# Optimization experiments

Measured on AMD Instinct MI355X. Metric: run time of the kernel, lower is better.

Reference implementation:

```python
import jax, jax.numpy as jnp
import numpy as np

T, B, I, H, O = 256, 64, 512, 1024, 256


def setup_inputs() -> dict:
    key = jax.random.key(0)
    ks = jax.random.split(key, 7)
    s_ih = 1.0 / np.sqrt(H)
    return {
        "x": jax.random.normal(ks[0], (T, B, I), dtype=jnp.float32),
        "W_ih": jax.random.uniform(ks[1], (4 * H, I), dtype=jnp.float32, minval=-s_ih, maxval=s_ih),
        "W_hh": jax.random.uniform(ks[2], (4 * H, H), dtype=jnp.float32, minval=-s_ih, maxval=s_ih),
        "b_ih": jax.random.uniform(ks[3], (4 * H,), dtype=jnp.float32, minval=-s_ih, maxval=s_ih),
        "b_hh": jax.random.uniform(ks[4], (4 * H,), dtype=jnp.float32, minval=-s_ih, maxval=s_ih),
        "fc_W": jax.random.uniform(ks[5], (O, H), dtype=jnp.float32, minval=-s_ih, maxval=s_ih),
        "fc_b": jax.random.uniform(ks[6], (O,), dtype=jnp.float32, minval=-s_ih, maxval=s_ih),
    }


def _lstm(x, W_ih, W_hh, b_ih, b_hh):
    # x: (T, B, I) seq-first, as PyTorch default. Gate order: i, f, g, o.
    Bsz = x.shape[1]
    Hh = W_hh.shape[1]
    # precompute input projections for all time steps: (T, B, 4H)
    xz = jnp.einsum('tbi,gi->tbg', x, W_ih) + b_ih + b_hh

    def step(carry, xz_t):
        h, c = carry
        z = xz_t + h @ W_hh.T  # (B, 4H)
        i, f, g, o = jnp.split(z, 4, axis=-1)
        i = jax.nn.sigmoid(i)
        f = jax.nn.sigmoid(f)
        g = jnp.tanh(g)
        o = jax.nn.sigmoid(o)
        c = f * c + i * g
        h = o * jnp.tanh(c)
        return (h, c), h

    h0 = jnp.zeros((Bsz, Hh), dtype=x.dtype)
    c0 = jnp.zeros((Bsz, Hh), dtype=x.dtype)
    _, hs = jax.lax.scan(step, (h0, c0), xz)
    return hs  # (T, B, H)


def reference(x, W_ih, W_hh, b_ih, b_hh, fc_W, fc_b):
    out = _lstm(x, W_ih, W_hh, b_ih, b_hh)  # (T, B, H)
    # Faithful to original: out[:, -1, :] indexes the LAST BATCH element
    # (seq-first layout), giving (T, H), then fc -> (T, O).
    last = out[:, -1, :]
    return last @ fc_W.T + fc_b
```

## Files before the change

kernel.cpp:

```cpp
#include <hip/hip_runtime.h>
#include <hip/hip_bf16.h>
#include <stdint.h>

#define T_STEPS 256
#define BATCH   64
#define IN_DIM  512
#define HID     1024
#define OUT_DIM 256
#define G4      4096
#define SENT    0x7FC07FC0u

__device__ __forceinline__ float bfbits2f(uint32_t b16) {
    return __uint_as_float(b16 << 16);
}
__device__ __forceinline__ uint32_t f2bfbits(float f) {
    uint32_t u = __float_as_uint(f);
    u += 0x7fffu + ((u >> 16) & 1u);
    return u >> 16;
}
__device__ __forceinline__ float fast_sigmoid(float x) {
    return 1.f / (1.f + __expf(-x));
}
__device__ __forceinline__ float fast_tanh(float x) {
    return 2.f / (1.f + __expf(-2.f * x)) - 1.f;
}

__global__ void init_sent(uint32_t* __restrict__ p, int n) {
    int i = blockIdx.x * 256 + threadIdx.x;
    if (i < n) p[i] = SENT;
}

template<bool ABF16>
__global__ __launch_bounds__(256) void gemm_bt(
    const void* __restrict__ Av, long lda,
    const float* __restrict__ Bw, int ldb,
    const float* __restrict__ bias1, const float* __restrict__ bias2,
    float* __restrict__ C, int ldc, int K)
{
    __shared__ float a_lds[64][68];
    __shared__ float w_lds[64][65];
    const int tid = threadIdx.x;
    const int m0 = blockIdx.y * 64, n0 = blockIdx.x * 64;
    const int kl = tid & 63, grp = tid >> 6;
    const int cc = tid & 31, r0 = (tid >> 5) * 8;

    float acc[16];
#pragma unroll
    for (int i = 0; i < 16; ++i) acc[i] = 0.f;

    for (int k0 = 0; k0 < K; k0 += 64) {
        __syncthreads();
#pragma unroll
        for (int i = 0; i < 16; ++i) {
            int r = grp + 4 * i;
            long ai = (long)(m0 + r) * lda + k0 + kl;
            float av = ABF16 ? bfbits2f(((const uint16_t*)Av)[ai])
                             : ((const float*)Av)[ai];
            a_lds[kl][r] = av;
            w_lds[kl][r] = Bw[(long)(n0 + r) * ldb + k0 + kl];
        }
        __syncthreads();
#pragma unroll 16
        for (int k = 0; k < 64; ++k) {
            float4 A0 = *(const float4*)&a_lds[k][r0];
            float4 A1 = *(const float4*)&a_lds[k][r0 + 4];
            float w0 = w_lds[k][cc], w1 = w_lds[k][cc + 32];
            float a[8] = {A0.x, A0.y, A0.z, A0.w, A1.x, A1.y, A1.z, A1.w};
#pragma unroll
            for (int i = 0; i < 8; ++i) {
                acc[i]     += a[i] * w0;
                acc[8 + i] += a[i] * w1;
            }
        }
    }
    float b0 = bias1[n0 + cc]      + (bias2 ? bias2[n0 + cc]      : 0.f);
    float b1 = bias1[n0 + cc + 32] + (bias2 ? bias2[n0 + cc + 32] : 0.f);
#pragma unroll
    for (int i = 0; i < 8; ++i) {
        C[(long)(m0 + r0 + i) * ldc + n0 + cc]      = acc[i]     + b0;
        C[(long)(m0 + r0 + i) * ldc + n0 + cc + 32] = acc[8 + i] + b1;
    }
}

__global__ __launch_bounds__(256) void lstm_rec(
    const float* __restrict__ W_hh,
    const float* __restrict__ xz,
    uint32_t* __restrict__ h_all)
{
    __shared__ float h_lds[HID];
    __shared__ float z_lds[16];

    const int g   = blockIdx.x;
    const int tid = threadIdx.x;
    const int kpart = tid & 15;
    const int row   = tid >> 4;
    const int gate  = row >> 2, ju = row & 3;
    const int grow  = gate * HID + g * 4 + ju;

    float w[64];
#pragma unroll
    for (int i = 0; i < 16; ++i) {
        int ch = (i + kpart) & 15;
        const float4 wv = *(const float4*)&W_hh[(long)grow * HID + kpart * 64 + ch * 4];
        w[4 * i + 0] = wv.x; w[4 * i + 1] = wv.y;
        w[4 * i + 2] = wv.z; w[4 * i + 3] = wv.w;
    }

    float c_state = 0.f;
    float xz_next = 0.f;
    if (kpart == 0) xz_next = xz[grow];

    for (int t = 0; t < T_STEPS; ++t) {
        if (t == 0) {
            float4 z4 = {0.f, 0.f, 0.f, 0.f};
            *(float4*)&h_lds[4 * tid] = z4;
        } else {
            const uint32_t* hsrc = h_all + (size_t)(t - 1) * 512;
            uint32_t v0, v1;
            do { v0 = __hip_atomic_load(&hsrc[2 * tid],     __ATOMIC_RELAXED, __HIP_MEMORY_SCOPE_AGENT); } while (v0 == SENT);
            do { v1 = __hip_atomic_load(&hsrc[2 * tid + 1], __ATOMIC_RELAXED, __HIP_MEMORY_SCOPE_AGENT); } while (v1 == SENT);
            float4 hv = { bfbits2f(v0 & 0xFFFFu), bfbits2f(v0 >> 16),
                          bfbits2f(v1 & 0xFFFFu), bfbits2f(v1 >> 16) };
            *(float4*)&h_lds[4 * tid] = hv;
        }
        __syncthreads();

        float xz_cur = 0.f;
        if (kpart == 0) {
            xz_cur = xz_next;
            int tn = (t + 1 < T_STEPS) ? t + 1 : t;
            xz_next = xz[(long)tn * G4 + grow];
        }

        float a0 = 0.f, a1 = 0.f, a2 = 0.f, a3 = 0.f;
#pragma unroll
        for (int i = 0; i < 16; ++i) {
            int ch = (i + kpart) & 15;
            float4 hv = *(const float4*)&h_lds[kpart * 64 + ch * 4];
            a0 += w[4 * i + 0] * hv.x;
            a1 += w[4 * i + 1] * hv.y;
            a2 += w[4 * i + 2] * hv.z;
            a3 += w[4 * i + 3] * hv.w;
        }
        float sum = (a0 + a1) + (a2 + a3);
        sum += __shfl_xor(sum, 1, 16);
        sum += __shfl_xor(sum, 2, 16);
        sum += __shfl_xor(sum, 4, 16);
        sum += __shfl_xor(sum, 8, 16);
        if (kpart == 0) z_lds[row] = sum + xz_cur;
        __syncthreads();

        if (tid < 4) {
            float zi = z_lds[tid], zf = z_lds[4 + tid];
            float zg = z_lds[8 + tid], zo = z_lds[12 + tid];
            float ii = fast_sigmoid(zi);
            float ff = fast_sigmoid(zf);
            float gg = fast_tanh(zg);
            float oo = fast_sigmoid(zo);
            c_state = ff * c_state + ii * gg;
            float h = oo * fast_tanh(c_state);
            uint32_t hb = f2bfbits(h);
            uint32_t other = __shfl_xor(hb, 1, 64);
            if ((tid & 1) == 0) {
                uint32_t dw = (hb & 0xFFFFu) | (other << 16);
                __hip_atomic_store(&h_all[(size_t)t * 512 + g * 2 + (tid >> 1)], dw,
                                   __ATOMIC_RELAXED, __HIP_MEMORY_SCOPE_AGENT);
            }
        }
    }
}

extern "C" void kernel_launch(void* const* d_in, const int* in_sizes, int n_in,
                              void* d_out, int out_size, void* d_ws, size_t ws_size,
                              hipStream_t stream) {
    const float* x    = (const float*)d_in[0];
    const float* W_ih = (const float*)d_in[1];
    const float* W_hh = (const float*)d_in[2];
    const float* b_ih = (const float*)d_in[3];
    const float* b_hh = (const float*)d_in[4];
    const float* fc_W = (const float*)d_in[5];
    const float* fc_b = (const float*)d_in[6];
    float* out = (float*)d_out;

    float*    xz    = (float*)d_ws;
    uint32_t* h_all = (uint32_t*)((char*)d_ws + (size_t)T_STEPS * G4 * 4);

    init_sent<<<(T_STEPS * HID / 2 + 255) / 256, 256, 0, stream>>>(h_all, T_STEPS * HID / 2);

    gemm_bt<false><<<dim3(G4 / 64, T_STEPS / 64), 256, 0, stream>>>(
        (const void*)(x + 63 * IN_DIM), (long)BATCH * IN_DIM,
        W_ih, IN_DIM, b_ih, b_hh, xz, G4, IN_DIM);

    lstm_rec<<<256, 256, 0, stream>>>(W_hh, xz, h_all);

    gemm_bt<true><<<dim3(OUT_DIM / 64, T_STEPS / 64), 256, 0, stream>>>(
        (const void*)h_all, HID, fc_W, HID, fc_b, nullptr, out, OUT_DIM, HID);
}
```

Baseline: 1.073 ms.

## Fuse input projection into recurrent kernel and tighten per-step sync

Removes the separate input-projection GEMM: each recurrent block computes its 16 gate rows of x·W_ih for all timesteps into LDS before the recurrence. Within each step, the gate sums are gathered with wave shuffles instead of a second __syncthreads, the h buffer is double-buffered, and each block writes its h values as individual 16-bit stores with cache-bypass bits. Consumers poll with one 64-bit load plus a sentinel check. This cuts one kernel launch, the xz round trip through global memory and a barrier per step, in exchange for redundant-free but serialized prologue work per block and stores that are not packed.

```diff
diff --git a/kernel.cpp b/kernel.cpp
--- a/kernel.cpp
+++ b/kernel.cpp
@@ -8,7 +8,8 @@
 #define HID     1024
 #define OUT_DIM 256
 #define G4      4096
-#define SENT    0x7FC07FC0u
+#define SENT32  0x7FC07FC0u
+#define SENT64  0x7FC07FC07FC07FC0ULL
 
 __device__ __forceinline__ float bfbits2f(uint32_t b16) {
     return __uint_as_float(b16 << 16);
@@ -24,17 +25,24 @@
 __device__ __forceinline__ float fast_tanh(float x) {
     return 2.f / (1.f + __expf(-2.f * x)) - 1.f;
 }
+__device__ __forceinline__ bool any_sent(uint64_t v) {
+    uint64_t x = v ^ SENT64;
+    return (((x - 0x0001000100010001ULL) & ~x) & 0x8000800080008000ULL) != 0ULL;
+}
+__device__ __forceinline__ uint64_t poll_load(const uint64_t* p) {
+    return __hip_atomic_load(p, __ATOMIC_RELAXED, __HIP_MEMORY_SCOPE_AGENT);
+}
 
 __global__ void init_sent(uint32_t* __restrict__ p, int n) {
     int i = blockIdx.x * 256 + threadIdx.x;
-    if (i < n) p[i] = SENT;
+    if (i < n) p[i] = SENT32;
 }
 
 template<bool ABF16>
 __global__ __launch_bounds__(256) void gemm_bt(
     const void* __restrict__ Av, long lda,
     const float* __restrict__ Bw, int ldb,
-    const float* __restrict__ bias1, const float* __restrict__ bias2,
+    const float* __restrict__ bias1,
     float* __restrict__ C, int ldc, int K)
 {
     __shared__ float a_lds[64][68];
@@ -73,8 +81,7 @@
             }
         }
     }
-    float b0 = bias1[n0 + cc]      + (bias2 ? bias2[n0 + cc]      : 0.f);
-    float b1 = bias1[n0 + cc + 32] + (bias2 ? bias2[n0 + cc + 32] : 0.f);
+    float b0 = bias1[n0 + cc], b1 = bias1[n0 + cc + 32];
 #pragma unroll
     for (int i = 0; i < 8; ++i) {
         C[(long)(m0 + r0 + i) * ldc + n0 + cc]      = acc[i]     + b0;
@@ -84,88 +91,126 @@
 
 __global__ __launch_bounds__(256) void lstm_rec(
     const float* __restrict__ W_hh,
-    const float* __restrict__ xz,
-    uint32_t* __restrict__ h_all)
+    const float* __restrict__ x,
+    const float* __restrict__ W_ih,
+    const float* __restrict__ b_ih,
+    const float* __restrict__ b_hh,
+    uint16_t* __restrict__ h_all)
 {
-    __shared__ float h_lds[HID];
-    __shared__ float z_lds[16];
-
-    const int g   = blockIdx.x;
-    const int tid = threadIdx.x;
+    __shared__ float h_lds[2][HID];
+    __shared__ float xz_lds[16][T_STEPS + 1];
+
+    const int g     = blockIdx.x;
+    const int tid   = threadIdx.x;
     const int kpart = tid & 15;
     const int row   = tid >> 4;
-    const int gate  = row >> 2, ju = row & 3;
+    const int ju    = row >> 2;
+    const int gate  = row & 3;
+    const int lane  = tid & 63;
     const int grow  = gate * HID + g * 4 + ju;
+
+    {
+        float wih[32];
+        const float* wp = W_ih + (long)grow * IN_DIM + kpart * 32;
+#pragma unroll
+        for (int i = 0; i < 8; ++i) {
+            float4 v = *(const float4*)(wp + 4 * i);
+            wih[4*i] = v.x; wih[4*i+1] = v.y; wih[4*i+2] = v.z; wih[4*i+3] = v.w;
+        }
+        float bsum = b_ih[grow] + b_hh[grow];
+        const float* xbase = x + (long)63 * IN_DIM + (long)kpart * 32;
+#pragma unroll 2
+        for (int t = 0; t < T_STEPS; ++t) {
+            const float* xp = xbase + (long)t * BATCH * IN_DIM;
+            float a0 = 0.f, a1 = 0.f, a2 = 0.f, a3 = 0.f;
+#pragma unroll
+            for (int i = 0; i < 8; ++i) {
+                float4 v = *(const float4*)(xp + 4 * i);
+                a0 += v.x * wih[4*i];   a1 += v.y * wih[4*i+1];
+                a2 += v.z * wih[4*i+2]; a3 += v.w * wih[4*i+3];
+            }
+            float acc = (a0 + a1) + (a2 + a3);
+            acc += __shfl_xor(acc, 1, 16);
+            acc += __shfl_xor(acc, 2, 16);
+            acc += __shfl_xor(acc, 4, 16);
+            acc += __shfl_xor(acc, 8, 16);
+            if (kpart == 0) xz_lds[row][t] = acc + bsum;
+        }
+    }
 
     float w[64];
 #pragma unroll
     for (int i = 0; i < 16; ++i) {
         int ch = (i + kpart) & 15;
-        const float4 wv = *(const float4*)&W_hh[(long)grow * HID + kpart * 64 + ch * 4];
-        w[4 * i + 0] = wv.x; w[4 * i + 1] = wv.y;
-        w[4 * i + 2] = wv.z; w[4 * i + 3] = wv.w;
-    }
+        float4 wv = *(const float4*)&W_hh[(long)grow * HID + kpart * 64 + ch * 4];
+        w[4*i] = wv.x; w[4*i+1] = wv.y; w[4*i+2] = wv.z; w[4*i+3] = wv.w;
+    }
+
+    {
+        float4 z4 = {0.f, 0.f, 0.f, 0.f};
+        *(float4*)&h_lds[0][4 * tid] = z4;
+    }
+    __syncthreads();
 
     float c_state = 0.f;
-    float xz_next = 0.f;
-    if (kpart == 0) xz_next = xz[grow];
+    float xz_next = xz_lds[row][0];
 
     for (int t = 0; t < T_STEPS; ++t) {
-        if (t == 0) {
-            float4 z4 = {0.f, 0.f, 0.f, 0.f};
-            *(float4*)&h_lds[4 * tid] = z4;
-        } else {
-            const uint32_t* hsrc = h_all + (size_t)(t - 1) * 512;
-            uint32_t v0, v1;
-            do { v0 = __hip_atomic_load(&hsrc[2 * tid],     __ATOMIC_RELAXED, __HIP_MEMORY_SCOPE_AGENT); } while (v0 == SENT);
-            do { v1 = __hip_atomic_load(&hsrc[2 * tid + 1], __ATOMIC_RELAXED, __HIP_MEMORY_SCOPE_AGENT); } while (v1 == SENT);
-            float4 hv = { bfbits2f(v0 & 0xFFFFu), bfbits2f(v0 >> 16),
-                          bfbits2f(v1 & 0xFFFFu), bfbits2f(v1 >> 16) };
-            *(float4*)&h_lds[4 * tid] = hv;
+        float* hb = h_lds[t & 1];
+        if (t > 0) {
+            const uint64_t* hsrc = (const uint64_t*)(h_all + (size_t)(t - 1) * HID);
+            uint64_t v = poll_load(&hsrc[tid]);
+            if (any_sent(v)) {
+                uint64_t a = poll_load(&hsrc[tid]);
+                uint64_t b = poll_load(&hsrc[tid]);
+                for (;;) {
+                    v = a; a = b; b = poll_load(&hsrc[tid]);
+                    if (!any_sent(v)) break;
+                }
+            }
+            float4 hv = { bfbits2f((uint32_t)(v        & 0xFFFFu)),
+                          bfbits2f((uint32_t)((v >> 16) & 0xFFFFu)),
+                          bfbits2f((uint32_t)((v >> 32) & 0xFFFFu)),
+                          bfbits2f((uint32_t)((v >> 48) & 0xFFFFu)) };
+            *(float4*)&hb[4 * tid] = hv;
         }
         __syncthreads();
 
-        float xz_cur = 0.f;
-        if (kpart == 0) {
-            xz_cur = xz_next;
-            int tn = (t + 1 < T_STEPS) ? t + 1 : t;
-            xz_next = xz[(long)tn * G4 + grow];
-        }
+        float xz_cur = xz_next;
+        int tn = (t + 1 < T_STEPS) ? t + 1 : t;
+        xz_next = xz_lds[row][tn];
 
         float a0 = 0.f, a1 = 0.f, a2 = 0.f, a3 = 0.f;
 #pragma unroll
         for (int i = 0; i < 16; ++i) {
-            int ch = (i + kpart) & 15;
-            float4 hv = *(const float4*)&h_lds[kpart * 64 + ch * 4];
-            a0 += w[4 * i + 0] * hv.x;
-            a1 += w[4 * i + 1] * hv.y;
-            a2 += w[4 * i + 2] * hv.z;
-            a3 += w[4 * i + 3] * hv.w;
+            float4 hv = *(const float4*)&hb[kpart * 64 + ((i + kpart) & 15) * 4];
+            a0 += w[4*i]   * hv.x;
+            a1 += w[4*i+1] * hv.y;
+            a2 += w[4*i+2] * hv.z;
+            a3 += w[4*i+3] * hv.w;
         }
         float sum = (a0 + a1) + (a2 + a3);
         sum += __shfl_xor(sum, 1, 16);
         sum += __shfl_xor(sum, 2, 16);
         sum += __shfl_xor(sum, 4, 16);
         sum += __shfl_xor(sum, 8, 16);
-        if (kpart == 0) z_lds[row] = sum + xz_cur;
-        __syncthreads();
-
-        if (tid < 4) {
-            float zi = z_lds[tid], zf = z_lds[4 + tid];
-            float zg = z_lds[8 + tid], zo = z_lds[12 + tid];
+        float z = sum + xz_cur;
+
+        float zi = __shfl(z,  0, 64);
+        float zf = __shfl(z, 16, 64);
+        float zg = __shfl(z, 32, 64);
+        float zo = __shfl(z, 48, 64);
+        if (lane == 0) {
             float ii = fast_sigmoid(zi);
             float ff = fast_sigmoid(zf);
             float gg = fast_tanh(zg);
             float oo = fast_sigmoid(zo);
             c_state = ff * c_state + ii * gg;
             float h = oo * fast_tanh(c_state);
-            uint32_t hb = f2bfbits(h);
-            uint32_t other = __shfl_xor(hb, 1, 64);
-            if ((tid & 1) == 0) {
-                uint32_t dw = (hb & 0xFFFFu) | (other << 16);
-                __hip_atomic_store(&h_all[(size_t)t * 512 + g * 2 + (tid >> 1)], dw,
-                                   __ATOMIC_RELAXED, __HIP_MEMORY_SCOPE_AGENT);
-            }
+            uint32_t hv32 = f2bfbits(h);
+            uint16_t* dst = h_all + (size_t)t * HID + g * 4 + ju;
+            asm volatile("global_store_short %0, %1, off sc0 sc1"
+                         :: "v"(dst), "v"(hv32) : "memory");
         }
     }
 }
@@ -182,17 +227,13 @@
     const float* fc_b = (const float*)d_in[6];
     float* out = (float*)d_out;
 
-    float*    xz    = (float*)d_ws;
-    uint32_t* h_all = (uint32_t*)((char*)d_ws + (size_t)T_STEPS * G4 * 4);
-
-    init_sent<<<(T_STEPS * HID / 2 + 255) / 256, 256, 0, stream>>>(h_all, T_STEPS * HID / 2);
-
-    gemm_bt<false><<<dim3(G4 / 64, T_STEPS / 64), 256, 0, stream>>>(
-        (const void*)(x + 63 * IN_DIM), (long)BATCH * IN_DIM,
-        W_ih, IN_DIM, b_ih, b_hh, xz, G4, IN_DIM);
-
-    lstm_rec<<<256, 256, 0, stream>>>(W_hh, xz, h_all);
+    uint16_t* h_all = (uint16_t*)d_ws;
+
+    init_sent<<<(T_STEPS * HID / 2 + 255) / 256, 256, 0, stream>>>(
+        (uint32_t*)h_all, T_STEPS * HID / 2);
+
+    lstm_rec<<<256, 256, 0, stream>>>(W_hh, x, W_ih, b_ih, b_hh, h_all);
 
     gemm_bt<true><<<dim3(OUT_DIM / 64, T_STEPS / 64), 256, 0, stream>>>(
-        (const void*)h_all, HID, fc_W, HID, fc_b, nullptr, out, OUT_DIM, HID);
-}
+        (const void*)h_all, HID, fc_W, HID, fc_b, out, OUT_DIM, HID);
+}
```

New measurement: 1.963 ms. 83.0% more time.
